# Optimization experiments

Measured on AMD Instinct MI355X. Metric: run time of the kernel, lower is better.

The kernel has to match this reference:

```python
import jax, jax.numpy as jnp
import numpy as np

P, C, D = 65536, 64, 256

def setup_inputs() -> dict:
    key = jax.random.key(0)
    k1, k2, k3, k4 = jax.random.split(key, 4)
    return {
        "protos1": jax.random.normal(k1, (P, D), dtype=jnp.float32),
        "protos2": jax.random.normal(k2, (P, D), dtype=jnp.float32),
        "W": jax.random.normal(k3, (D, D), dtype=jnp.float32) / np.float32(np.sqrt(D)),
        "b": jax.random.normal(k4, (D,), dtype=jnp.float32),
        "num_classes": C,
    }

def _pairwise_dist(x, y):
    # x: (C, n, D), y: (C, m, D) -> squared-euclidean-style dists (C, n, m)
    xs = jnp.sum(x * x, axis=-1)[:, :, None]
    ys = jnp.sum(y * y, axis=-1)[:, None, :]
    return xs + ys - 2.0 * jnp.einsum('cid,cjd->cij', x, y)

def reference(protos1, protos2, W, b, num_classes):
    nc = int(num_classes)
    d = protos1.shape[-1]
    # prototypes[c::num_classes] for all c at once: (P,D) -> (P//C, C, D) -> (C, P//C, D)
    p1 = protos1.reshape(-1, nc, d).transpose(1, 0, 2)
    p2 = protos2.reshape(-1, nc, d).transpose(1, 0, 2)
    # transition: nn.Linear -> x @ W.T + b ; inverse: (x - b) @ inv(W.T)
    p2_inv = (p2 - b) @ jnp.linalg.inv(W.T)
    p1_fwd = p1 @ W.T + b
    a = _pairwise_dist(p1, p2_inv)          # (C, n, n)
    bb = _pairwise_dist(p2, p1_fwd)         # (C, n, n)
    proto_losses_source = jnp.mean(jnp.min(a, axis=2), axis=1)   # (C,)
    proto_losses_target = jnp.mean(jnp.min(bb, axis=2), axis=1)  # (C,)
    return jnp.stack([proto_losses_source, proto_losses_target])  # (2, C)
```

## Files before the change

kernel.cpp:

```cpp
#include <hip/hip_runtime.h>

#define D 256
#define NC 64

using u16 = unsigned short;
using u32 = unsigned int;

typedef __attribute__((ext_vector_type(8))) short bfv8;
typedef __attribute__((ext_vector_type(4))) float f32x4;
typedef __attribute__((ext_vector_type(2))) int v2i;

__device__ __forceinline__ float bf2f(u32 u) {
  union { u32 i; float f; } v; v.i = u << 16; return v.f;
}
__device__ __forceinline__ u16 f2bf(float f) {
  union { float f; u32 i; } v; v.f = f;
  u32 x = v.i;
  return (u16)((x + 0x7FFFu + ((x >> 16) & 1u)) >> 16);
}
__device__ __forceinline__ u32 pk2(float a, float b) {
  return (u32)f2bf(a) | ((u32)f2bf(b) << 16);
}
__device__ __forceinline__ size_t cmrow(int g) {
  return (size_t)(((g & 63) << 10) | (g >> 6));
}

__device__ __forceinline__ void gload_lds16(const void* src, void* dst) {
  __builtin_amdgcn_global_load_lds(
      (const __attribute__((address_space(1))) void*)src,
      (__attribute__((address_space(3))) void*)dst, 16, 0, 0);
}

#define PH_LDS 71168
#define DIST_LDS 66560

__device__ void gj_body(const float* __restrict__ W, float* __restrict__ IW,
                        char* smem) {
  float (*Ml)[20]    = (float(*)[20])smem;
  float (*Arow)[256] = (float(*)[256])(smem + 20480);
  float (*G)[256]    = (float(*)[256])(smem + 36864);
  u16*  Gfrag        = (u16*)(smem + 53248);
  float (*Pinv)[20]  = (float(*)[20])(smem + 69888);
  const int t = threadIdx.x, w = t >> 6, l = t & 63;
  const int lj = l & 15, lh = l >> 4;
  const int r0 = 16 * w;
  const bool lo32 = (l < 32);

  f32x4 x[16];
#pragma unroll
  for (int ct = 0; ct < 16; ++ct)
#pragma unroll
    for (int reg = 0; reg < 4; ++reg)
      x[ct][reg] = W[(size_t)(r0 + 4 * lh + reg) * D + 16 * ct + lj];

  for (int s = 0; s < 16; ++s) {
#pragma unroll
    for (int ct = 0; ct < 16; ++ct)
      if (ct == s)
#pragma unroll
        for (int reg = 0; reg < 4; ++reg)
          Ml[r0 + 4 * lh + reg][lj] = x[ct][reg];
    if (w == s) {
#pragma unroll
      for (int ct = 0; ct < 16; ++ct)
#pragma unroll
        for (int reg = 0; reg < 4; ++reg)
          Arow[4 * lh + reg][16 * ct + lj] = x[ct][reg];
    }
    bfv8 afr;
    {
      const int row = r0 + lj;
      float4 f0 = *(const float4*)&Ml[row][8 * (lh & 1)];
      float4 f1 = *(const float4*)&Ml[row][8 * (lh & 1) + 4];
      const float fv[8] = {f0.x, f0.y, f0.z, f0.w, f1.x, f1.y, f1.z, f1.w};
      union { bfv8 v; u16 e[8]; } A;
      if (lh < 2) {
#pragma unroll
        for (int e = 0; e < 8; ++e) A.e[e] = f2bf(-fv[e]);
      } else {
#pragma unroll
        for (int e = 0; e < 8; ++e) {
          const float hi = bf2f(f2bf(fv[e]));
          A.e[e] = f2bf(-(fv[e] - hi));
        }
      }
      afr = A.v;
    }
    __syncthreads();
    if (t < 16) {
      float p[16];
      {
        float4 rr0 = *(const float4*)&Ml[16 * s + t][0];
        float4 rr1 = *(const float4*)&Ml[16 * s + t][4];
        float4 rr2 = *(const float4*)&Ml[16 * s + t][8];
        float4 rr3 = *(const float4*)&Ml[16 * s + t][12];
        p[0] = rr0.x; p[1] = rr0.y; p[2] = rr0.z; p[3] = rr0.w;
        p[4] = rr1.x; p[5] = rr1.y; p[6] = rr1.z; p[7] = rr1.w;
        p[8] = rr2.x; p[9] = rr2.y; p[10] = rr2.z; p[11] = rr2.w;
        p[12] = rr3.x; p[13] = rr3.y; p[14] = rr3.z; p[15] = rr3.w;
      }
#pragma unroll
      for (int pp = 0; pp < 16; ++pp) {
        float u[16];
#pragma unroll
        for (int j = 0; j < 16; ++j)
          u[j] = __int_as_float(__builtin_amdgcn_readlane(__float_as_int(p[j]), pp));
        const float pv = u[pp];
        const float d = 1.0f / pv;
        if (t == pp) {
#pragma unroll
          for (int j = 0; j < 16; ++j) p[j] = u[j] * d;
          p[pp] = d;
        } else {
          const float md = p[pp] * d;
          u[pp] = pv + 1.0f;
#pragma unroll
          for (int j = 0; j < 16; ++j) p[j] = fmaf(-md, u[j], p[j]);
        }
      }
#pragma unroll
      for (int j = 0; j < 16; ++j) Pinv[t][j] = p[j];
    }
    __syncthreads();
    {
      const bool inC = ((l >> 2) == s);
      const int co = (l & 3) << 2;
      const int gct = l >> 2;
      const int kk = w;
      float4 g = make_float4(0.f, 0.f, 0.f, 0.f);
#pragma unroll
      for (int q = 0; q < 16; ++q) {
        const float pv = Pinv[kk][q];
        const float4 av = *(const float4*)&Arow[q][4 * l];
        g.x = fmaf(pv, av.x, g.x); g.y = fmaf(pv, av.y, g.y);
        g.z = fmaf(pv, av.z, g.z); g.w = fmaf(pv, av.w, g.w);
      }
      if (inC) {
        g.x = Pinv[kk][co + 0] + (kk == co + 0 ? 1.f : 0.f);
        g.y = Pinv[kk][co + 1] + (kk == co + 1 ? 1.f : 0.f);
        g.z = Pinv[kk][co + 2] + (kk == co + 2 ? 1.f : 0.f);
        g.w = Pinv[kk][co + 3] + (kk == co + 3 ? 1.f : 0.f);
      }
      *(float4*)&G[kk][4 * l] = g;
      const int e0 = kk & 7;
      const int lbase = 16 * (kk >> 3);
      const float gv[4] = {g.x, g.y, g.z, g.w};
#pragma unroll
      for (int cc = 0; cc < 4; ++cc) {
        const int cl = 4 * (l & 3) + cc;
        const u16 hi = f2bf(gv[cc]);
        const u16 lo = f2bf(gv[cc] - bf2f(hi));
        Gfrag[gct * 520 + (lbase + cl) * 8 + e0] = hi;
        Gfrag[gct * 520 + (32 + lbase + cl) * 8 + e0] = lo;
      }
    }
    __syncthreads();
    if (w != s) {
#pragma unroll
      for (int ct = 0; ct < 16; ++ct) {
        union { bfv8 v; uint4 u; } B1, B2;
        B1.v = *(const bfv8*)&Gfrag[ct * 520 + l * 8];
#if __has_builtin(__builtin_amdgcn_permlane32_swap)
        {
          v2i r;
          r = __builtin_amdgcn_permlane32_swap((int)B1.u.x, (int)B1.u.x, false, false);
          B2.u.x = lo32 ? (u32)r.y : (u32)r.x;
          r = __builtin_amdgcn_permlane32_swap((int)B1.u.y, (int)B1.u.y, false, false);
          B2.u.y = lo32 ? (u32)r.y : (u32)r.x;
          r = __builtin_amdgcn_permlane32_swap((int)B1.u.z, (int)B1.u.z, false, false);
          B2.u.z = lo32 ? (u32)r.y : (u32)r.x;
          r = __builtin_amdgcn_permlane32_swap((int)B1.u.w, (int)B1.u.w, false, false);
          B2.u.w = lo32 ? (u32)r.y : (u32)r.x;
        }
#else
        B2.v = *(const bfv8*)&Gfrag[ct * 520 + (l ^ 32) * 8];
#endif
        x[ct] = __builtin_amdgcn_mfma_f32_16x16x32_bf16(afr, B1.v, x[ct], 0, 0, 0);
        x[ct] = __builtin_amdgcn_mfma_f32_16x16x32_bf16(afr, B2.v, x[ct], 0, 0, 0);
      }
    } else {
#pragma unroll
      for (int ct = 0; ct < 16; ++ct) {
        if (ct == s) {
#pragma unroll
          for (int reg = 0; reg < 4; ++reg)
            x[ct][reg] = Pinv[4 * lh + reg][lj];
        } else {
#pragma unroll
          for (int reg = 0; reg < 4; ++reg)
            x[ct][reg] = G[4 * lh + reg][16 * ct + lj];
        }
      }
    }
    __syncthreads();
  }
#pragma unroll
  for (int ct = 0; ct < 16; ++ct)
#pragma unroll
    for (int reg = 0; reg < 4; ++reg)
      IW[(size_t)(r0 + 4 * lh + reg) * D + 16 * ct + lj] = x[ct][reg];
}

template <int MODE, bool WRITE_NRM>
__device__ void prep_body(const float* __restrict__ Ain,
                          const u16* __restrict__ Brows,
                          const float* __restrict__ biasv,
                          u16* __restrict__ Out, float* __restrict__ nrm,
                          float* __restrict__ nfp, int it, char* smem) {
  const int tx = threadIdx.x, ww = tx >> 6, l = tx & 63;
  const int mw = ww >> 3, nw = ww & 7, l4 = l >> 4, lm = l & 15;
  char* Ab = smem;
  float* nfpart = (float*)(smem + 65536);

  bfv8 bfr[2][8];
#pragma unroll
  for (int nf2 = 0; nf2 < 2; ++nf2)
#pragma unroll
    for (int ks = 0; ks < 8; ++ks)
      bfr[nf2][ks] = *(const bfv8*)(Brows +
          (size_t)(nw * 32 + nf2 * 16 + lm) * D + ks * 32 + l4 * 8);

  {
    const int r = tx >> 3, sg = tx & 7;
    const float* arow = Ain + (size_t)(it * 128 + r) * D + sg * 32;
    float ss = 0.f;
#pragma unroll
    for (int g2 = 0; g2 < 4; ++g2) {
      float4 v0 = *(const float4*)(arow + g2 * 8);
      float4 v1 = *(const float4*)(arow + g2 * 8 + 4);
      ss = fmaf(v0.x, v0.x, fmaf(v0.y, v0.y, fmaf(v0.z, v0.z, fmaf(v0.w, v0.w, ss))));
      ss = fmaf(v1.x, v1.x, fmaf(v1.y, v1.y, fmaf(v1.z, v1.z, fmaf(v1.w, v1.w, ss))));
      uint4 w4;
      w4.x = pk2(v0.x, v0.y); w4.y = pk2(v0.z, v0.w);
      w4.z = pk2(v1.x, v1.y); w4.w = pk2(v1.z, v1.w);
      *(uint4*)(Ab + (sg * 8 + (r >> 4)) * 1024 + ((r & 15) + g2 * 16) * 16) = w4;
    }
    ss += __shfl_xor(ss, 1, 64);
    ss += __shfl_xor(ss, 2, 64);
    ss += __shfl_xor(ss, 4, 64);
    if (WRITE_NRM && sg == 0) nrm[cmrow(it * 128 + r)] = ss;
  }
  __syncthreads();

  const bfv8* A8 = (const bfv8*)Ab;
  f32x4 acc[4][2];
#pragma unroll
  for (int mf = 0; mf < 4; ++mf) {
    acc[mf][0] = f32x4{0.f, 0.f, 0.f, 0.f};
    acc[mf][1] = f32x4{0.f, 0.f, 0.f, 0.f};
  }
#pragma unroll
  for (int ks = 0; ks < 8; ++ks)
#pragma unroll
    for (int mf = 0; mf < 4; ++mf) {
      bfv8 a = A8[(ks * 8 + mw * 4 + mf) * 64 + l];
      acc[mf][0] = __builtin_amdgcn_mfma_f32_16x16x32_bf16(a, bfr[0][ks], acc[mf][0], 0, 0, 0);
      acc[mf][1] = __builtin_amdgcn_mfma_f32_16x16x32_bf16(a, bfr[1][ks], acc[mf][1], 0, 0, 0);
    }

  float bias[2];
  if (MODE == 0) {
#pragma unroll
    for (int nf2 = 0; nf2 < 2; ++nf2)
      bias[nf2] = biasv[nw * 32 + nf2 * 16 + lm];
  } else {
#pragma unroll
    for (int nf2 = 0; nf2 < 2; ++nf2) {
      float pd = 0.f;
#pragma unroll
      for (int ks = 0; ks < 8; ++ks) {
        float4 b0 = *(const float4*)(biasv + ks * 32 + l4 * 8);
        float4 b1 = *(const float4*)(biasv + ks * 32 + l4 * 8 + 4);
        pd = fmaf(b0.x, bf2f((u16)bfr[nf2][ks][0]), pd);
        pd = fmaf(b0.y, bf2f((u16)bfr[nf2][ks][1]), pd);
        pd = fmaf(b0.z, bf2f((u16)bfr[nf2][ks][2]), pd);
        pd = fmaf(b0.w, bf2f((u16)bfr[nf2][ks][3]), pd);
        pd = fmaf(b1.x, bf2f((u16)bfr[nf2][ks][4]), pd);
        pd = fmaf(b1.y, bf2f((u16)bfr[nf2][ks][5]), pd);
        pd = fmaf(b1.z, bf2f((u16)bfr[nf2][ks][6]), pd);
        pd = fmaf(b1.w, bf2f((u16)bfr[nf2][ks][7]), pd);
      }
      pd += __shfl_xor(pd, 16, 64);
      pd += __shfl_xor(pd, 32, 64);
      bias[nf2] = -pd;
    }
  }

#pragma unroll
  for (int mf = 0; mf < 4; ++mf)
#pragma unroll
    for (int rr = 0; rr < 4; ++rr) {
      const int g = it * 128 + mw * 64 + mf * 16 + l4 * 4 + rr;
      const size_t orow = cmrow(g) * D;
      float v2 = 0.f;
#pragma unroll
      for (int nf2 = 0; nf2 < 2; ++nf2) {
        const float v = acc[mf][nf2][rr] + bias[nf2];
        const u16 hv = f2bf(v);
        Out[orow + nw * 32 + nf2 * 16 + lm] = hv;
        const float vr = bf2f(hv);
        v2 = fmaf(vr, vr, v2);
      }
      v2 += __shfl_xor(v2, 1, 64);
      v2 += __shfl_xor(v2, 2, 64);
      v2 += __shfl_xor(v2, 4, 64);
      v2 += __shfl_xor(v2, 8, 64);
      if (lm == 0) nfpart[nw * 128 + mw * 64 + mf * 16 + l4 * 4 + rr] = v2;
    }
  __syncthreads();
  if (tx < 128) {
    float s = 0.f;
#pragma unroll
    for (int q = 0; q < 8; ++q) s += nfpart[q * 128 + tx];
    nfp[cmrow(it * 128 + tx)] = s;
  }
}

__device__ void norms_role(const float* __restrict__ p2, float* __restrict__ n2,
                           int idx) {
  const int tx = threadIdx.x, q = tx & 3;
#pragma unroll
  for (int rep = 0; rep < 8; ++rep) {
    const int g = idx * 2048 + rep * 256 + (tx >> 2);
    const float* row = p2 + (size_t)g * D + q * 64;
    float ss = 0.f;
#pragma unroll
    for (int g2 = 0; g2 < 16; ++g2) {
      float4 v = *(const float4*)(row + g2 * 4);
      ss = fmaf(v.x, v.x, fmaf(v.y, v.y, fmaf(v.z, v.z, fmaf(v.w, v.w, ss))));
    }
    ss += __shfl_xor(ss, 1, 64);
    ss += __shfl_xor(ss, 2, 64);
    if (q == 0) n2[cmrow(g)] = ss;
  }
}

__global__ __launch_bounds__(1024, 1) void phase1_kernel(
    const float* __restrict__ p1, const float* __restrict__ p2,
    const float* __restrict__ W, const u16* __restrict__ Wb,
    const float* __restrict__ bv, u16* __restrict__ Fb,
    float* __restrict__ n1, float* __restrict__ n2,
    float* __restrict__ nf, float* __restrict__ IWa) {
  extern __shared__ char smem[];
  const int b = blockIdx.x;
  if (b == 0) {
    gj_body(W, IWa, smem);
  } else if (b <= 512) {
    prep_body<0, true>(p1, Wb, bv, Fb, n1, nf, b - 1, smem);
  } else {
    norms_role(p2, n2, b - 513);
  }
}

__global__ __launch_bounds__(1024, 1) void phase3_kernel(
    const float* __restrict__ p2, const u16* __restrict__ IWb,
    const float* __restrict__ bv, u16* __restrict__ Qb,
    float* __restrict__ nq) {
  extern __shared__ char smem[];
  prep_body<1, false>(p2, IWb, bv, Qb, nullptr, nq, blockIdx.x, smem);
}

__global__ __launch_bounds__(256) void nr_mult_bf16(const float* __restrict__ X,
                                                    const float* __restrict__ R,
                                                    u16* __restrict__ Yb) {
  __shared__ float xrow[D];
  const int i = blockIdx.x, j = threadIdx.x;
  xrow[j] = X[i * D + j];
  __syncthreads();
  float acc = 0.f;
#pragma unroll 8
  for (int k = 0; k < D; ++k) acc = fmaf(xrow[k], R[k * D + j], acc);
  Yb[i * D + j] = f2bf(acc);
}

__global__ __launch_bounds__(256) void wconv(const float* __restrict__ W,
                                             u16* __restrict__ Wb) {
  const int i = blockIdx.x * 256 + threadIdx.x;
  Wb[i] = f2bf(W[i]);
}

template <int DIR>
__device__ void dist_body(const float* __restrict__ Ain,
                          const u16* __restrict__ Bin,
                          const float* __restrict__ nA,
                          const float* __restrict__ nB,
                          float* __restrict__ partial, int bid, char* smem) {
  const int lb = (bid & 7) * 64 + (bid >> 3);
  const int c = lb >> 3, it = lb & 7;
  const int tx = threadIdx.x, wid = tx >> 6, l = tx & 63;
  const int l4 = l >> 4, lm = l & 15;

  auto issue_b = [&](int half, int jt) {
    const size_t base = ((size_t)(c << 10) + jt * 128) * D;
#pragma unroll
    for (int jf = 0; jf < 8; ++jf) {
      const u16* src = Bin + base + (size_t)(jf * 16 + lm) * D
                       + half * 128 + wid * 32 + l4 * 8;
      gload_lds16(src, smem + half * 32768 + (wid * 8 + jf) * 1024);
    }
  };

  issue_b(0, 0);
  bfv8 afr[2][8];
  const float* abase = Ain + ((size_t)(it * 128 + wid * 32) * NC + c) * D;
#pragma unroll
  for (int m = 0; m < 2; ++m)
#pragma unroll
    for (int ks = 0; ks < 8; ++ks) {
      const float* ap = abase + (size_t)(m * 16 + lm) * (NC * D) + ks * 32 + l4 * 8;
      float4 v0 = *(const float4*)(ap);
      float4 v1 = *(const float4*)(ap + 4);
      union { bfv8 v; uint4 u; } cv;
      cv.u.x = pk2(v0.x, v0.y); cv.u.y = pk2(v0.z, v0.w);
      cv.u.z = pk2(v1.x, v1.y); cv.u.w = pk2(v1.z, v1.w);
      afr[m][ks] = cv.v;
    }
  float na[2][4];
#pragma unroll
  for (int m = 0; m < 2; ++m)
#pragma unroll
    for (int rr = 0; rr < 4; ++rr)
      na[m][rr] = nA[(c << 10) + it * 128 + wid * 32 + m * 16 + l4 * 4 + rr];
  float minv[2][4];
#pragma unroll
  for (int m = 0; m < 2; ++m)
#pragma unroll
    for (int rr = 0; rr < 4; ++rr) minv[m][rr] = 3.0e38f;
  __syncthreads();

  const bfv8* lds8 = (const bfv8*)smem;
  for (int jt = 0; jt < 8; ++jt) {
    f32x4 acc[2][8];
#pragma unroll
    for (int m = 0; m < 2; ++m)
#pragma unroll
      for (int n = 0; n < 8; ++n) acc[m][n] = f32x4{0.f, 0.f, 0.f, 0.f};
    float nbv[8];
#pragma unroll
    for (int n = 0; n < 8; ++n)
      nbv[n] = nB[(c << 10) + jt * 128 + n * 16 + lm];
    issue_b(1, jt);
#pragma unroll
    for (int ks = 0; ks < 4; ++ks) {
      bfv8 bb[8];
#pragma unroll
      for (int n = 0; n < 8; ++n) bb[n] = lds8[(ks * 8 + n) * 64 + l];
#pragma unroll
      for (int m = 0; m < 2; ++m)
#pragma unroll
        for (int n = 0; n < 8; ++n)
          acc[m][n] = __builtin_amdgcn_mfma_f32_16x16x32_bf16(afr[m][ks], bb[n], acc[m][n], 0, 0, 0);
    }
    __syncthreads();
    if (jt < 7) issue_b(0, jt + 1);
#pragma unroll
    for (int ks = 4; ks < 8; ++ks) {
      bfv8 bb[8];
#pragma unroll
      for (int n = 0; n < 8; ++n) bb[n] = lds8[2048 + ((ks - 4) * 8 + n) * 64 + l];
#pragma unroll
      for (int m = 0; m < 2; ++m)
#pragma unroll
        for (int n = 0; n < 8; ++n)
          acc[m][n] = __builtin_amdgcn_mfma_f32_16x16x32_bf16(afr[m][ks], bb[n], acc[m][n], 0, 0, 0);
    }
#pragma unroll
    for (int m = 0; m < 2; ++m)
#pragma unroll
      for (int n = 0; n < 8; ++n)
#pragma unroll
        for (int rr = 0; rr < 4; ++rr) {
          const float dd = na[m][rr] + nbv[n] - 2.0f * acc[m][n][rr];
          minv[m][rr] = fminf(minv[m][rr], dd);
        }
    __syncthreads();
  }
  float* red = (float*)(smem + 65536);
#pragma unroll
  for (int m = 0; m < 2; ++m)
#pragma unroll
    for (int rr = 0; rr < 4; ++rr) {
      float mm = minv[m][rr];
      mm = fminf(mm, __shfl_xor(mm, 1, 64));
      mm = fminf(mm, __shfl_xor(mm, 2, 64));
      mm = fminf(mm, __shfl_xor(mm, 4, 64));
      mm = fminf(mm, __shfl_xor(mm, 8, 64));
      if (lm == 0) red[wid * 32 + m * 16 + l4 * 4 + rr] = mm;
    }
  __syncthreads();
  if (tx < 128) {
    float v = red[tx];
#pragma unroll
    for (int off = 32; off; off >>= 1) v += __shfl_xor(v, off, 64);
    if ((tx & 63) == 0) red[128 + (tx >> 6)] = v;
  }
  __syncthreads();
  if (tx == 0) partial[(c << 4) | (DIR << 3) | it] = red[128] + red[129];
}

__global__ __launch_bounds__(256, 2) void phase2_kernel(
    const float* __restrict__ p2, const u16* __restrict__ Fb,
    const float* __restrict__ n2, const float* __restrict__ nf,
    const float* __restrict__ W, const float* __restrict__ IWa,
    float* __restrict__ Rt, float* __restrict__ partial) {
  extern __shared__ char smem[];
  const int b = blockIdx.x;
  if (b < 512) {
    dist_body<1>(p2, Fb, n2, nf, partial, b, smem);
  } else {
    float* wrow = (float*)smem;
    const int i = b - 512, j = threadIdx.x;
    wrow[j] = W[i * D + j];
    __syncthreads();
    float acc = 0.f;
#pragma unroll 8
    for (int k = 0; k < D; ++k) acc = fmaf(wrow[k], IWa[k * D + j], acc);
    Rt[i * D + j] = (i == j ? 2.0f : 0.0f) - acc;
  }
}

__global__ __launch_bounds__(256, 2) void dist0_kernel(
    const float* __restrict__ p1, const u16* __restrict__ Qb,
    const float* __restrict__ n1, const float* __restrict__ nq,
    float* __restrict__ partial) {
  extern __shared__ char smem[];
  dist_body<0>(p1, Qb, n1, nq, partial, blockIdx.x, smem);
}

__global__ void finalize_kernel(const float* __restrict__ partial,
                                float* __restrict__ out) {
  const int tx = threadIdx.x;
  if (tx >= 128) return;
  const int dir = tx >> 6, c = tx & 63;
  float s = 0.f;
#pragma unroll
  for (int it = 0; it < 8; ++it) s += partial[(c << 4) | (dir << 3) | it];
  out[dir * 64 + c] = s * (1.0f / 1024.0f);
}

extern "C" void kernel_launch(void* const* d_in, const int* in_sizes, int n_in,
                              void* d_out, int out_size, void* d_ws, size_t ws_size,
                              hipStream_t stream) {
  const float* p1 = (const float*)d_in[0];
  const float* p2 = (const float*)d_in[1];
  const float* W  = (const float*)d_in[2];
  const float* bv = (const float*)d_in[3];
  float* out = (float*)d_out;
  char* ws = (char*)d_ws;
  float* n1   = (float*)(ws);
  float* n2   = (float*)(ws + (256 << 10));
  float* nf   = (float*)(ws + (512 << 10));
  float* nq   = (float*)(ws + (768 << 10));
  float* partial = (float*)(ws + (1024 << 10));
  u16* Wb  = (u16*)(ws + (1032 << 10));
  u16* IWb = (u16*)(ws + (1160 << 10));
  float* IWa = (float*)(ws + (1288 << 10));
  float* Rt  = (float*)(ws + (1544 << 10));
  u16* Fb  = (u16*)(ws + (2048 << 10));
  u16* Qb  = (u16*)(ws + (2048 << 10) + (32u << 20));

  hipFuncSetAttribute((const void*)phase1_kernel,
                      hipFuncAttributeMaxDynamicSharedMemorySize, PH_LDS);
  hipFuncSetAttribute((const void*)phase2_kernel,
                      hipFuncAttributeMaxDynamicSharedMemorySize, DIST_LDS);
  hipFuncSetAttribute((const void*)phase3_kernel,
                      hipFuncAttributeMaxDynamicSharedMemorySize, PH_LDS);
  hipFuncSetAttribute((const void*)dist0_kernel,
                      hipFuncAttributeMaxDynamicSharedMemorySize, DIST_LDS);

  wconv<<<256, 256, 0, stream>>>(W, Wb);
  phase1_kernel<<<545, 1024, PH_LDS, stream>>>(p1, p2, W, Wb, bv, Fb,
                                               n1, n2, nf, IWa);
  phase2_kernel<<<768, 256, DIST_LDS, stream>>>(p2, Fb, n2, nf, W, IWa,
                                                Rt, partial);
  nr_mult_bf16<<<256, 256, 0, stream>>>(IWa, Rt, IWb);
  phase3_kernel<<<512, 1024, PH_LDS, stream>>>(p2, IWb, bv, Qb, nq);
  dist0_kernel<<<512, 256, DIST_LDS, stream>>>(p1, Qb, n1, nq, partial);
  finalize_kernel<<<1, 128, 0, stream>>>(partial, out);
}
```

Baseline: 297.6 us.

## Fuse projection GEMM with distance-min computation, streaming raw bf16 prototypes

Restructures the pipeline so each projection block keeps its transformed 128-row tile in LDS and computes distances against the other side's bf16-converted prototypes directly. This removes the round trip of writing the transformed tensors to global memory and reading them back, and drops two separate kernels. Raw prototypes are converted to bf16 with their norms in a pre-pass, partial row minima go to a global buffer, and a new final kernel reduces them. The fused kernel uses 1024 threads at one block per CU with double-buffered chunk loads. Each output block now re-streams a whole class's 1024 rows, and the min reduction syncs the block after every chunk, which may lower MFMA utilisation compared with the old dedicated distance kernel.

```diff
diff --git a/kernel.cpp b/kernel.cpp
--- a/kernel.cpp
+++ b/kernel.cpp
@@ -31,8 +31,8 @@
       (__attribute__((address_space(3))) void*)dst, 16, 0, 0);
 }
 
-#define PH_LDS 71168
-#define DIST_LDS 66560
+#define GJ_LDS 71168
+#define DISTP_LDS 135680
 
 __device__ void gj_body(const float* __restrict__ W, float* __restrict__ IW,
                         char* smem) {
@@ -201,16 +201,56 @@
       IW[(size_t)(r0 + 4 * lh + reg) * D + 16 * ct + lj] = x[ct][reg];
 }
 
-template <int MODE, bool WRITE_NRM>
-__device__ void prep_body(const float* __restrict__ Ain,
-                          const u16* __restrict__ Brows,
-                          const float* __restrict__ biasv,
-                          u16* __restrict__ Out, float* __restrict__ nrm,
-                          float* __restrict__ nfp, int it, char* smem) {
+__device__ void convnorm_role(const float* __restrict__ P, u16* __restrict__ Pb,
+                              float* __restrict__ nrm, int blk) {
+  const int tx = threadIdx.x;
+  const int r = tx >> 2, q = tx & 3;
+  const int g = blk * 256 + r;
+  const float* src = P + (size_t)g * D + q * 64;
+  u16* dst = Pb + cmrow(g) * D + q * 64;
+  float ss = 0.f;
+#pragma unroll
+  for (int g4 = 0; g4 < 8; ++g4) {
+    float4 v0 = *(const float4*)(src + g4 * 8);
+    float4 v1 = *(const float4*)(src + g4 * 8 + 4);
+    ss = fmaf(v0.x, v0.x, fmaf(v0.y, v0.y, fmaf(v0.z, v0.z, fmaf(v0.w, v0.w, ss))));
+    ss = fmaf(v1.x, v1.x, fmaf(v1.y, v1.y, fmaf(v1.z, v1.z, fmaf(v1.w, v1.w, ss))));
+    uint4 w4;
+    w4.x = pk2(v0.x, v0.y); w4.y = pk2(v0.z, v0.w);
+    w4.z = pk2(v1.x, v1.y); w4.w = pk2(v1.z, v1.w);
+    *(uint4*)(dst + g4 * 8) = w4;
+  }
+  ss += __shfl_xor(ss, 1, 64);
+  ss += __shfl_xor(ss, 2, 64);
+  if (q == 0) nrm[cmrow(g)] = ss;
+}
+
+template <int MODE>
+__device__ void distp_body(const float* __restrict__ Pj,
+                           const u16* __restrict__ Brows,
+                           const float* __restrict__ biasv,
+                           const u16* __restrict__ Pib,
+                           const float* __restrict__ nB,
+                           float* __restrict__ pmind, int bid, char* smem) {
+  const int lb = (bid & 7) * 64 + (bid >> 3);
+  const int c = lb >> 3, jt = lb & 7;
   const int tx = threadIdx.x, ww = tx >> 6, l = tx & 63;
   const int mw = ww >> 3, nw = ww & 7, l4 = l >> 4, lm = l & 15;
   char* Ab = smem;
-  float* nfpart = (float*)(smem + 65536);
+  char* Bb = smem + 65536;
+  float* nfpart = (float*)(smem + 131072);
+  float* minbuf = (float*)(smem + 131072);
+  float* nAb = (float*)(smem + 135168);
+
+  auto issue_chunk = [&](int buf, int ch) {
+#pragma unroll
+    for (int u = 0; u < 2; ++u) {
+      const int chunk = ww * 2 + u, ks = chunk >> 2, n = chunk & 3;
+      const u16* src = Pib + ((size_t)(c << 10) + ch * 64 + n * 16 + lm) * D
+                       + ks * 32 + l4 * 8;
+      gload_lds16(src, Bb + buf * 32768 + chunk * 1024);
+    }
+  };
 
   bfv8 bfr[2][8];
 #pragma unroll
@@ -219,29 +259,20 @@
     for (int ks = 0; ks < 8; ++ks)
       bfr[nf2][ks] = *(const bfv8*)(Brows +
           (size_t)(nw * 32 + nf2 * 16 + lm) * D + ks * 32 + l4 * 8);
-
   {
     const int r = tx >> 3, sg = tx & 7;
-    const float* arow = Ain + (size_t)(it * 128 + r) * D + sg * 32;
-    float ss = 0.f;
+    const float* arow = Pj + ((size_t)(jt * 128 + r) * NC + c) * D + sg * 32;
 #pragma unroll
     for (int g2 = 0; g2 < 4; ++g2) {
       float4 v0 = *(const float4*)(arow + g2 * 8);
       float4 v1 = *(const float4*)(arow + g2 * 8 + 4);
-      ss = fmaf(v0.x, v0.x, fmaf(v0.y, v0.y, fmaf(v0.z, v0.z, fmaf(v0.w, v0.w, ss))));
-      ss = fmaf(v1.x, v1.x, fmaf(v1.y, v1.y, fmaf(v1.z, v1.z, fmaf(v1.w, v1.w, ss))));
       uint4 w4;
       w4.x = pk2(v0.x, v0.y); w4.y = pk2(v0.z, v0.w);
       w4.z = pk2(v1.x, v1.y); w4.w = pk2(v1.z, v1.w);
       *(uint4*)(Ab + (sg * 8 + (r >> 4)) * 1024 + ((r & 15) + g2 * 16) * 16) = w4;
     }
-    ss += __shfl_xor(ss, 1, 64);
-    ss += __shfl_xor(ss, 2, 64);
-    ss += __shfl_xor(ss, 4, 64);
-    if (WRITE_NRM && sg == 0) nrm[cmrow(it * 128 + r)] = ss;
-  }
-  __syncthreads();
-
+  }
+  __syncthreads();
   const bfv8* A8 = (const bfv8*)Ab;
   f32x4 acc[4][2];
 #pragma unroll
@@ -257,7 +288,6 @@
       acc[mf][0] = __builtin_amdgcn_mfma_f32_16x16x32_bf16(a, bfr[0][ks], acc[mf][0], 0, 0, 0);
       acc[mf][1] = __builtin_amdgcn_mfma_f32_16x16x32_bf16(a, bfr[1][ks], acc[mf][1], 0, 0, 0);
     }
-
   float bias[2];
   if (MODE == 0) {
 #pragma unroll
@@ -285,19 +315,21 @@
       bias[nf2] = -pd;
     }
   }
-
+  __syncthreads();
+  issue_chunk(0, 0);
+  u16* tile = (u16*)Ab;
 #pragma unroll
   for (int mf = 0; mf < 4; ++mf)
 #pragma unroll
     for (int rr = 0; rr < 4; ++rr) {
-      const int g = it * 128 + mw * 64 + mf * 16 + l4 * 4 + rr;
-      const size_t orow = cmrow(g) * D;
+      const int j = mw * 64 + mf * 16 + l4 * 4 + rr;
       float v2 = 0.f;
 #pragma unroll
       for (int nf2 = 0; nf2 < 2; ++nf2) {
         const float v = acc[mf][nf2][rr] + bias[nf2];
         const u16 hv = f2bf(v);
-        Out[orow + nw * 32 + nf2 * 16 + lm] = hv;
+        tile[(((nw * 8 + mw * 4 + mf) << 6) + ((nf2 * 2 + (lm >> 3)) << 4)
+              + l4 * 4 + rr) * 8 + (lm & 7)] = hv;
         const float vr = bf2f(hv);
         v2 = fmaf(vr, vr, v2);
       }
@@ -305,59 +337,101 @@
       v2 += __shfl_xor(v2, 2, 64);
       v2 += __shfl_xor(v2, 4, 64);
       v2 += __shfl_xor(v2, 8, 64);
-      if (lm == 0) nfpart[nw * 128 + mw * 64 + mf * 16 + l4 * 4 + rr] = v2;
+      if (lm == 0) nfpart[nw * 128 + j] = v2;
     }
   __syncthreads();
   if (tx < 128) {
     float s = 0.f;
 #pragma unroll
     for (int q = 0; q < 8; ++q) s += nfpart[q * 128 + tx];
-    nfp[cmrow(it * 128 + tx)] = s;
-  }
-}
-
-__device__ void norms_role(const float* __restrict__ p2, float* __restrict__ n2,
-                           int idx) {
-  const int tx = threadIdx.x, q = tx & 3;
-#pragma unroll
-  for (int rep = 0; rep < 8; ++rep) {
-    const int g = idx * 2048 + rep * 256 + (tx >> 2);
-    const float* row = p2 + (size_t)g * D + q * 64;
-    float ss = 0.f;
-#pragma unroll
-    for (int g2 = 0; g2 < 16; ++g2) {
-      float4 v = *(const float4*)(row + g2 * 4);
-      ss = fmaf(v.x, v.x, fmaf(v.y, v.y, fmaf(v.z, v.z, fmaf(v.w, v.w, ss))));
-    }
-    ss += __shfl_xor(ss, 1, 64);
-    ss += __shfl_xor(ss, 2, 64);
-    if (q == 0) n2[cmrow(g)] = ss;
-  }
-}
-
-__global__ __launch_bounds__(1024, 1) void phase1_kernel(
-    const float* __restrict__ p1, const float* __restrict__ p2,
-    const float* __restrict__ W, const u16* __restrict__ Wb,
-    const float* __restrict__ bv, u16* __restrict__ Fb,
-    float* __restrict__ n1, float* __restrict__ n2,
-    float* __restrict__ nf, float* __restrict__ IWa) {
+    nAb[tx] = s;
+  }
+  __syncthreads();
+  const int jw = ww >> 1, iw = ww & 1;
+  const float* nBc = nB + (c << 10);
+  const size_t obase = (size_t)(c * 8 + jt) * 1024;
+  for (int ch = 0; ch < 16; ++ch) {
+    if (ch < 15) issue_chunk((ch + 1) & 1, ch + 1);
+    const bfv8* B8 = (const bfv8*)(Bb + (ch & 1) * 32768);
+    f32x4 a2[2];
+    a2[0] = f32x4{0.f, 0.f, 0.f, 0.f};
+    a2[1] = f32x4{0.f, 0.f, 0.f, 0.f};
+#pragma unroll
+    for (int ks = 0; ks < 8; ++ks) {
+      bfv8 a = A8[(ks * 8 + jw) * 64 + l];
+#pragma unroll
+      for (int t = 0; t < 2; ++t) {
+        bfv8 b = B8[(ks * 4 + iw * 2 + t) * 64 + l];
+        a2[t] = __builtin_amdgcn_mfma_f32_16x16x32_bf16(a, b, a2[t], 0, 0, 0);
+      }
+    }
+#pragma unroll
+    for (int t = 0; t < 2; ++t) {
+      const int ig = iw * 2 + t;
+      const float nb = nBc[ch * 64 + ig * 16 + lm];
+      float mm = 3.0e38f;
+#pragma unroll
+      for (int rr = 0; rr < 4; ++rr) {
+        const int j = jw * 16 + l4 * 4 + rr;
+        const float dd = nb + nAb[j] - 2.0f * a2[t][rr];
+        mm = fminf(mm, dd);
+      }
+      mm = fminf(mm, __shfl_xor(mm, 16, 64));
+      mm = fminf(mm, __shfl_xor(mm, 32, 64));
+      if (l4 == 0) minbuf[jw * 64 + ig * 16 + lm] = mm;
+    }
+    __syncthreads();
+    if (tx < 64) {
+      float m = minbuf[tx];
+#pragma unroll
+      for (int q = 1; q < 8; ++q) m = fminf(m, minbuf[q * 64 + tx]);
+      pmind[obase + ch * 64 + tx] = m;
+    }
+    __syncthreads();
+  }
+}
+
+__global__ __launch_bounds__(1024, 1) void k0_kernel(
+    const float* __restrict__ p2, u16* __restrict__ p2b,
+    float* __restrict__ n2, const float* __restrict__ W,
+    u16* __restrict__ Wb) {
+  if (blockIdx.x < 256) {
+    convnorm_role(p2, p2b, n2, blockIdx.x);
+  } else {
+    const int t = threadIdx.x;
+#pragma unroll
+    for (int k = 0; k < 64; ++k) Wb[k * 1024 + t] = f2bf(W[k * 1024 + t]);
+  }
+}
+
+__global__ __launch_bounds__(1024, 1) void k1_kernel(
+    const float* __restrict__ p1, const float* __restrict__ W,
+    const u16* __restrict__ Wb, const float* __restrict__ bv,
+    const u16* __restrict__ p2b, const float* __restrict__ n2,
+    float* __restrict__ pmin1, float* __restrict__ IWa,
+    u16* __restrict__ p1b, float* __restrict__ n1) {
   extern __shared__ char smem[];
   const int b = blockIdx.x;
   if (b == 0) {
     gj_body(W, IWa, smem);
   } else if (b <= 512) {
-    prep_body<0, true>(p1, Wb, bv, Fb, n1, nf, b - 1, smem);
+    distp_body<0>(p1, Wb, bv, p2b, n2, pmin1, b - 1, smem);
   } else {
-    norms_role(p2, n2, b - 513);
-  }
-}
-
-__global__ __launch_bounds__(1024, 1) void phase3_kernel(
-    const float* __restrict__ p2, const u16* __restrict__ IWb,
-    const float* __restrict__ bv, u16* __restrict__ Qb,
-    float* __restrict__ nq) {
-  extern __shared__ char smem[];
-  prep_body<1, false>(p2, IWb, bv, Qb, nullptr, nq, blockIdx.x, smem);
+    convnorm_role(p1, p1b, n1, b - 513);
+  }
+}
+
+__global__ __launch_bounds__(256) void nr_residual(const float* __restrict__ W,
+                                                   const float* __restrict__ X,
+                                                   float* __restrict__ R) {
+  __shared__ float wrow[D];
+  const int i = blockIdx.x, j = threadIdx.x;
+  wrow[j] = W[i * D + j];
+  __syncthreads();
+  float acc = 0.f;
+#pragma unroll 8
+  for (int k = 0; k < D; ++k) acc = fmaf(wrow[k], X[k * D + j], acc);
+  R[i * D + j] = (i == j ? 2.0f : 0.0f) - acc;
 }
 
 __global__ __launch_bounds__(256) void nr_mult_bf16(const float* __restrict__ X,
@@ -373,169 +447,34 @@
   Yb[i * D + j] = f2bf(acc);
 }
 
-__global__ __launch_bounds__(256) void wconv(const float* __restrict__ W,
-                                             u16* __restrict__ Wb) {
-  const int i = blockIdx.x * 256 + threadIdx.x;
-  Wb[i] = f2bf(W[i]);
-}
-
-template <int DIR>
-__device__ void dist_body(const float* __restrict__ Ain,
-                          const u16* __restrict__ Bin,
-                          const float* __restrict__ nA,
-                          const float* __restrict__ nB,
-                          float* __restrict__ partial, int bid, char* smem) {
-  const int lb = (bid & 7) * 64 + (bid >> 3);
-  const int c = lb >> 3, it = lb & 7;
-  const int tx = threadIdx.x, wid = tx >> 6, l = tx & 63;
-  const int l4 = l >> 4, lm = l & 15;
-
-  auto issue_b = [&](int half, int jt) {
-    const size_t base = ((size_t)(c << 10) + jt * 128) * D;
-#pragma unroll
-    for (int jf = 0; jf < 8; ++jf) {
-      const u16* src = Bin + base + (size_t)(jf * 16 + lm) * D
-                       + half * 128 + wid * 32 + l4 * 8;
-      gload_lds16(src, smem + half * 32768 + (wid * 8 + jf) * 1024);
-    }
-  };
-
-  issue_b(0, 0);
-  bfv8 afr[2][8];
-  const float* abase = Ain + ((size_t)(it * 128 + wid * 32) * NC + c) * D;
-#pragma unroll
-  for (int m = 0; m < 2; ++m)
-#pragma unroll
-    for (int ks = 0; ks < 8; ++ks) {
-      const float* ap = abase + (size_t)(m * 16 + lm) * (NC * D) + ks * 32 + l4 * 8;
-      float4 v0 = *(const float4*)(ap);
-      float4 v1 = *(const float4*)(ap + 4);
-      union { bfv8 v; uint4 u; } cv;
-      cv.u.x = pk2(v0.x, v0.y); cv.u.y = pk2(v0.z, v0.w);
-      cv.u.z = pk2(v1.x, v1.y); cv.u.w = pk2(v1.z, v1.w);
-      afr[m][ks] = cv.v;
-    }
-  float na[2][4];
-#pragma unroll
-  for (int m = 0; m < 2; ++m)
-#pragma unroll
-    for (int rr = 0; rr < 4; ++rr)
-      na[m][rr] = nA[(c << 10) + it * 128 + wid * 32 + m * 16 + l4 * 4 + rr];
-  float minv[2][4];
-#pragma unroll
-  for (int m = 0; m < 2; ++m)
-#pragma unroll
-    for (int rr = 0; rr < 4; ++rr) minv[m][rr] = 3.0e38f;
-  __syncthreads();
-
-  const bfv8* lds8 = (const bfv8*)smem;
-  for (int jt = 0; jt < 8; ++jt) {
-    f32x4 acc[2][8];
-#pragma unroll
-    for (int m = 0; m < 2; ++m)
-#pragma unroll
-      for (int n = 0; n < 8; ++n) acc[m][n] = f32x4{0.f, 0.f, 0.f, 0.f};
-    float nbv[8];
-#pragma unroll
-    for (int n = 0; n < 8; ++n)
-      nbv[n] = nB[(c << 10) + jt * 128 + n * 16 + lm];
-    issue_b(1, jt);
-#pragma unroll
-    for (int ks = 0; ks < 4; ++ks) {
-      bfv8 bb[8];
-#pragma unroll
-      for (int n = 0; n < 8; ++n) bb[n] = lds8[(ks * 8 + n) * 64 + l];
-#pragma unroll
-      for (int m = 0; m < 2; ++m)
-#pragma unroll
-        for (int n = 0; n < 8; ++n)
-          acc[m][n] = __builtin_amdgcn_mfma_f32_16x16x32_bf16(afr[m][ks], bb[n], acc[m][n], 0, 0, 0);
-    }
-    __syncthreads();
-    if (jt < 7) issue_b(0, jt + 1);
-#pragma unroll
-    for (int ks = 4; ks < 8; ++ks) {
-      bfv8 bb[8];
-#pragma unroll
-      for (int n = 0; n < 8; ++n) bb[n] = lds8[2048 + ((ks - 4) * 8 + n) * 64 + l];
-#pragma unroll
-      for (int m = 0; m < 2; ++m)
-#pragma unroll
-        for (int n = 0; n < 8; ++n)
-          acc[m][n] = __builtin_amdgcn_mfma_f32_16x16x32_bf16(afr[m][ks], bb[n], acc[m][n], 0, 0, 0);
-    }
-#pragma unroll
-    for (int m = 0; m < 2; ++m)
-#pragma unroll
-      for (int n = 0; n < 8; ++n)
-#pragma unroll
-        for (int rr = 0; rr < 4; ++rr) {
-          const float dd = na[m][rr] + nbv[n] - 2.0f * acc[m][n][rr];
-          minv[m][rr] = fminf(minv[m][rr], dd);
-        }
-    __syncthreads();
-  }
-  float* red = (float*)(smem + 65536);
-#pragma unroll
-  for (int m = 0; m < 2; ++m)
-#pragma unroll
-    for (int rr = 0; rr < 4; ++rr) {
-      float mm = minv[m][rr];
-      mm = fminf(mm, __shfl_xor(mm, 1, 64));
-      mm = fminf(mm, __shfl_xor(mm, 2, 64));
-      mm = fminf(mm, __shfl_xor(mm, 4, 64));
-      mm = fminf(mm, __shfl_xor(mm, 8, 64));
-      if (lm == 0) red[wid * 32 + m * 16 + l4 * 4 + rr] = mm;
-    }
-  __syncthreads();
-  if (tx < 128) {
-    float v = red[tx];
-#pragma unroll
-    for (int off = 32; off; off >>= 1) v += __shfl_xor(v, off, 64);
-    if ((tx & 63) == 0) red[128 + (tx >> 6)] = v;
-  }
-  __syncthreads();
-  if (tx == 0) partial[(c << 4) | (DIR << 3) | it] = red[128] + red[129];
-}
-
-__global__ __launch_bounds__(256, 2) void phase2_kernel(
-    const float* __restrict__ p2, const u16* __restrict__ Fb,
-    const float* __restrict__ n2, const float* __restrict__ nf,
-    const float* __restrict__ W, const float* __restrict__ IWa,
-    float* __restrict__ Rt, float* __restrict__ partial) {
+__global__ __launch_bounds__(1024, 1) void k3_kernel(
+    const float* __restrict__ p2, const u16* __restrict__ IWb,
+    const float* __restrict__ bv, const u16* __restrict__ p1b,
+    const float* __restrict__ n1, float* __restrict__ pmin0) {
   extern __shared__ char smem[];
-  const int b = blockIdx.x;
-  if (b < 512) {
-    dist_body<1>(p2, Fb, n2, nf, partial, b, smem);
-  } else {
-    float* wrow = (float*)smem;
-    const int i = b - 512, j = threadIdx.x;
-    wrow[j] = W[i * D + j];
-    __syncthreads();
-    float acc = 0.f;
-#pragma unroll 8
-    for (int k = 0; k < D; ++k) acc = fmaf(wrow[k], IWa[k * D + j], acc);
-    Rt[i * D + j] = (i == j ? 2.0f : 0.0f) - acc;
-  }
-}
-
-__global__ __launch_bounds__(256, 2) void dist0_kernel(
-    const float* __restrict__ p1, const u16* __restrict__ Qb,
-    const float* __restrict__ n1, const float* __restrict__ nq,
-    float* __restrict__ partial) {
-  extern __shared__ char smem[];
-  dist_body<0>(p1, Qb, n1, nq, partial, blockIdx.x, smem);
-}
-
-__global__ void finalize_kernel(const float* __restrict__ partial,
-                                float* __restrict__ out) {
-  const int tx = threadIdx.x;
-  if (tx >= 128) return;
-  const int dir = tx >> 6, c = tx & 63;
+  distp_body<1>(p2, IWb, bv, p1b, n1, pmin0, blockIdx.x, smem);
+}
+
+__global__ __launch_bounds__(256) void final_kernel(const float* __restrict__ pmin,
+                                                    float* __restrict__ out) {
+  __shared__ float ws4[4];
+  const int dc = blockIdx.x, tx = threadIdx.x;
+  const float* base = pmin + (size_t)dc * 8192;
   float s = 0.f;
 #pragma unroll
-  for (int it = 0; it < 8; ++it) s += partial[(c << 4) | (dir << 3) | it];
-  out[dir * 64 + c] = s * (1.0f / 1024.0f);
+  for (int t = 0; t < 4; ++t) {
+    const int i = t * 256 + tx;
+    float m = base[i];
+#pragma unroll
+    for (int j = 1; j < 8; ++j) m = fminf(m, base[j * 1024 + i]);
+    s += m;
+  }
+#pragma unroll
+  for (int off = 32; off; off >>= 1) s += __shfl_xor(s, off, 64);
+  if ((tx & 63) == 0) ws4[tx >> 6] = s;
+  __syncthreads();
+  if (tx == 0)
+    out[dc] = (ws4[0] + ws4[1] + ws4[2] + ws4[3]) * (1.0f / 1024.0f);
 }
 
 extern "C" void kernel_launch(void* const* d_in, const int* in_sizes, int n_in,
@@ -547,34 +486,28 @@
   const float* bv = (const float*)d_in[3];
   float* out = (float*)d_out;
   char* ws = (char*)d_ws;
-  float* n1   = (float*)(ws);
-  float* n2   = (float*)(ws + (256 << 10));
-  float* nf   = (float*)(ws + (512 << 10));
-  float* nq   = (float*)(ws + (768 << 10));
-  float* partial = (float*)(ws + (1024 << 10));
-  u16* Wb  = (u16*)(ws + (1032 << 10));
-  u16* IWb = (u16*)(ws + (1160 << 10));
-  float* IWa = (float*)(ws + (1288 << 10));
-  float* Rt  = (float*)(ws + (1544 << 10));
-  u16* Fb  = (u16*)(ws + (2048 << 10));
-  u16* Qb  = (u16*)(ws + (2048 << 10) + (32u << 20));
-
-  hipFuncSetAttribute((const void*)phase1_kernel,
-                      hipFuncAttributeMaxDynamicSharedMemorySize, PH_LDS);
-  hipFuncSetAttribute((const void*)phase2_kernel,
-                      hipFuncAttributeMaxDynamicSharedMemorySize, DIST_LDS);
-  hipFuncSetAttribute((const void*)phase3_kernel,
-                      hipFuncAttributeMaxDynamicSharedMemorySize, PH_LDS);
-  hipFuncSetAttribute((const void*)dist0_kernel,
-                      hipFuncAttributeMaxDynamicSharedMemorySize, DIST_LDS);
-
-  wconv<<<256, 256, 0, stream>>>(W, Wb);
-  phase1_kernel<<<545, 1024, PH_LDS, stream>>>(p1, p2, W, Wb, bv, Fb,
-                                               n1, n2, nf, IWa);
-  phase2_kernel<<<768, 256, DIST_LDS, stream>>>(p2, Fb, n2, nf, W, IWa,
-                                                Rt, partial);
+  float* n1  = (float*)(ws);
+  float* n2  = (float*)(ws + (256 << 10));
+  u16* Wb    = (u16*)(ws + (512 << 10));
+  u16* IWb   = (u16*)(ws + (640 << 10));
+  float* IWa = (float*)(ws + (768 << 10));
+  float* Rt  = (float*)(ws + (1024 << 10));
+  float* pmin = (float*)(ws + (1280 << 10));
+  u16* p1b   = (u16*)(ws + (6u << 20));
+  u16* p2b   = (u16*)(ws + (38u << 20));
+  float* pmin0 = pmin;
+  float* pmin1 = pmin + 524288;
+
+  hipFuncSetAttribute((const void*)k1_kernel,
+                      hipFuncAttributeMaxDynamicSharedMemorySize, DISTP_LDS);
+  hipFuncSetAttribute((const void*)k3_kernel,
+                      hipFuncAttributeMaxDynamicSharedMemorySize, DISTP_LDS);
+
+  k0_kernel<<<257, 1024, 0, stream>>>(p2, p2b, n2, W, Wb);
+  k1_kernel<<<769, 1024, DISTP_LDS, stream>>>(p1, W, Wb, bv, p2b, n2,
+                                              pmin1, IWa, p1b, n1);
+  nr_residual<<<256, 256, 0, stream>>>(W, IWa, Rt);
   nr_mult_bf16<<<256, 256, 0, stream>>>(IWa, Rt, IWb);
-  phase3_kernel<<<512, 1024, PH_LDS, stream>>>(p2, IWb, bv, Qb, nq);
-  dist0_kernel<<<512, 256, DIST_LDS, stream>>>(p1, Qb, n1, nq, partial);
-  finalize_kernel<<<1, 128, 0, stream>>>(partial, out);
-}
+  k3_kernel<<<512, 1024, DISTP_LDS, stream>>>(p2, IWb, bv, p1b, n1, pmin0);
+  final_kernel<<<128, 256, 0, stream>>>(pmin, out);
+}
```

New measurement: 281.9 us. 5.3% less time.
